# Optimization experiments

Measured on AMD Instinct MI355X. Metric: run time of the kernel, lower is better.

Reference implementation:

```python
import jax, jax.numpy as jnp
import numpy as np

TEMP = 0.1      # temperature
REG = 0.1       # ot_reg
MAX_ITER = 100  # Sinkhorn-style scaling iterations (original early-stops on tol; fixed-point is identical post-convergence)

B, D, N_PER = 64, 128, 512  # examples, embed dim, nodes/tokens per example


def _normalize(x):
    # torch F.normalize(dim=1): x / max(||x||, eps)
    n = jnp.linalg.norm(x, axis=1, keepdims=True)
    return x / jnp.maximum(n, 1e-12)


def setup_inputs() -> dict:
    key = jax.random.key(0)
    k0, k1, k2, k3 = jax.random.split(key, 4)
    N = B * N_PER
    return {
        "struct_global": jax.random.normal(k0, (B, D), jnp.float32),
        "seq_global": jax.random.normal(k1, (B, D), jnp.float32),
        "struct_nodes": jax.random.normal(k2, (N, D), jnp.float32),
        "seq_tokens": jax.random.normal(k3, (N, D), jnp.float32),
        # sorted, equal-size segments: example i owns rows [i*N_PER, (i+1)*N_PER)
        "batch_idx": jnp.repeat(jnp.arange(B), N_PER),
    }


def _global_nt_xent(struct_emb, seq_emb):
    s = _normalize(struct_emb)
    q = _normalize(seq_emb)
    sim = (s @ q.T) / TEMP                      # [B, B]
    loss_i = -jnp.mean(jnp.diagonal(jax.nn.log_softmax(sim, axis=1)))
    loss_j = -jnp.mean(jnp.diagonal(jax.nn.log_softmax(sim.T, axis=1)))
    return (loss_i + loss_j) / 2.0


def _local_ot_loss(struct_nodes, seq_tokens):
    # batch_idx is sorted equal-size segments -> dense batched reshape
    sn = _normalize(struct_nodes).reshape(B, N_PER, D)
    st = _normalize(seq_tokens).reshape(B, N_PER, D)
    C = -jnp.einsum('bnd,bmd->bnm', sn, st)     # [B, n, m] cost
    n = m = N_PER
    # Original detaches cost to numpy before OT -> transport plan P is a constant w.r.t. grads
    C_sg = jax.lax.stop_gradient(C)
    P0 = jnp.exp(-C_sg / REG)
    a = jnp.full((B, n), 1.0 / n, C.dtype)
    b = jnp.full((B, m), 1.0 / m, C.dtype)

    def body(_, uv):
        u, v = uv
        # Jacobi-style update: both use the previous (u, v), matching the source
        u_new = a / jnp.einsum('bnm,bm->bn', P0, v)
        v_new = b / jnp.einsum('bnm,bn->bm', P0, u)
        u_new = jnp.nan_to_num(u_new, nan=1.0 / n, posinf=1.0 / n, neginf=1.0 / n)
        v_new = jnp.nan_to_num(v_new, nan=1.0 / m, posinf=1.0 / m, neginf=1.0 / m)
        return (u_new, v_new)

    u, v = jax.lax.fori_loop(0, MAX_ITER, body, (a, b))  # init u=1/n, v=1/m as in source
    P = u[:, :, None] * P0 * v[:, None, :]      # diag(u) @ P0 @ diag(v)
    total = jnp.sum(P * C)                      # grads flow through C only
    return total / B


def reference(struct_global, seq_global, struct_nodes, seq_tokens, batch_idx):
    global_loss = _global_nt_xent(struct_global, seq_global)
    local_loss = _local_ot_loss(struct_nodes, seq_tokens)
    total_loss = global_loss + local_loss
    return (global_loss, local_loss, total_loss)
```

## Files before the change

kernel.cpp:

```cpp
#include <hip/hip_runtime.h>
#include <cstdint>
#include <cmath>

#define NB_EX 64
#define DIMD 128
#define NP 512
constexpr float MARG = 1.0f / 512.0f;

__device__ __forceinline__ float bf2f_lo(unsigned w) { return __uint_as_float(w << 16); }
__device__ __forceinline__ float bf2f_hi(unsigned w) { return __uint_as_float(w & 0xFFFF0000u); }
__device__ __forceinline__ unsigned short f2bf(float f) {
    unsigned u = __float_as_uint(f);
    u += 0x7FFFu + ((u >> 16) & 1u);
    return (unsigned short)(u >> 16);
}
__device__ __forceinline__ float wred64(float v) {
#pragma unroll
    for (int m = 1; m < 64; m <<= 1) v += __shfl_xor(v, m, 64);
    return v;
}

__device__ __forceinline__ unsigned l2_sc0_load(const unsigned* p) {
    unsigned v;
    asm volatile("global_load_dword %0, %1, off sc0\n\ts_waitcnt vmcnt(0)"
                 : "=v"(v) : "v"(p) : "memory");
    return v;
}

__device__ __forceinline__ int self_detect(const unsigned* probe, int t) {
    __shared__ int sd_cnt[4];
    unsigned w = probe[t];
    unsigned e = (w >> 7) & 0xFFu;
    unsigned long long m = __ballot(e >= 110u && e <= 130u);
    if ((t & 63) == 0) sd_cnt[t >> 6] = __popcll(m);
    __syncthreads();
    int c = sd_cnt[0] + sd_cnt[1] + sd_cnt[2] + sd_cnt[3];
    __syncthreads();
    return c >= 128;
}

#define O_SIMG   0
#define O_RNAN   16384
#define O_RNBN   147456
#define O_COLP   278528
#define O_COLPIF 2375680
#define O_P0     4472832

__global__ void k_rnormAB(const void* anr, const void* bnr, float* rnan, float* rnbn) {
    int t = threadIdx.x;
    int flag = self_detect((const unsigned*)anr, t);
    int gr  = blockIdx.x * 4 + (t >> 6);
    int lane = t & 63;
    const void* in = (gr < 32768) ? anr : bnr;
    float* rn      = (gr < 32768) ? rnan : rnbn;
    int row = gr & 32767;
    float f0, f1;
    if (flag) {
        unsigned w = ((const unsigned*)in)[row * 64 + lane];
        f0 = bf2f_lo(w); f1 = bf2f_hi(w);
    } else {
        float2 v = ((const float2*)in)[row * 64 + lane];
        f0 = v.x; f1 = v.y;
    }
    float ss = wred64(f0 * f0 + f1 * f1);
    if (lane == 0) rn[row] = 1.0f / fmaxf(sqrtf(ss), 1e-12f);
}

__global__ void k_simg(const void* sgr, const void* qgr, float* simg) {
    __shared__ float rls[128];
    int t = threadIdx.x;
    int flag = self_detect((const unsigned*)sgr, t);
    int w = t >> 6, lane = t & 63;
    for (int rr = 0; rr < 32; rr++) {
        int ri = w * 32 + rr;
        const void* base = (ri < 64) ? sgr : qgr;
        int row = ri & 63;
        float f0, f1;
        if (flag) {
            unsigned wd = ((const unsigned*)base)[row * 64 + lane];
            f0 = bf2f_lo(wd); f1 = bf2f_hi(wd);
        } else {
            float2 v = ((const float2*)base)[row * 64 + lane];
            f0 = v.x; f1 = v.y;
        }
        float ss = wred64(f0 * f0 + f1 * f1);
        if (lane == 0) rls[ri] = 1.0f / fmaxf(sqrtf(ss), 1e-12f);
    }
    __syncthreads();
    int g = blockIdx.x * 256 + t;
    int i = g >> 6, j = g & 63;
    float dot = 0.f;
    if (flag) {
        const unsigned* a = (const unsigned*)sgr + i * 64;
        const unsigned* b = (const unsigned*)qgr + j * 64;
        for (int k = 0; k < 64; k++) {
            unsigned wa = a[k], wb = b[k];
            dot += bf2f_lo(wa) * bf2f_lo(wb);
            dot += bf2f_hi(wa) * bf2f_hi(wb);
        }
    } else {
        const float4* a = (const float4*)sgr + i * 32;
        const float4* b = (const float4*)qgr + j * 32;
        for (int k = 0; k < 32; k++) {
            float4 x = a[k], y = b[k];
            dot += x.x * y.x + x.y * y.y + x.z * y.z + x.w * y.w;
        }
    }
    simg[g] = dot * rls[i] * rls[64 + j] * 10.0f;
}

__global__ void k_gloss(const float* __restrict__ simg, float* outf) {
    __shared__ float red[64];
    int i = threadIdx.x;
    if (i < 64) {
        float m = -1e30f;
        for (int j = 0; j < 64; j++) m = fmaxf(m, simg[i * 64 + j]);
        float se = 0.f;
        for (int j = 0; j < 64; j++) se += expf(simg[i * 64 + j] - m);
        float rl = simg[i * 64 + i] - (m + logf(se));
        float m2 = -1e30f;
        for (int j = 0; j < 64; j++) m2 = fmaxf(m2, simg[j * 64 + i]);
        float se2 = 0.f;
        for (int j = 0; j < 64; j++) se2 += expf(simg[j * 64 + i] - m2);
        float cl = simg[i * 64 + i] - (m2 + logf(se2));
        red[i] = rl + cl;
    }
    __syncthreads();
    if (i == 0) {
        float s = 0.f;
        for (int k = 0; k < 64; k++) s += red[k];
        float g = -s / 128.0f;
        outf[0] = g;
        outf[1] = 0.0f;
        outf[2] = g;
    }
}

__global__ void k_build(const void* anr, const void* bnr, const float* rnan, const float* rnbn,
                        unsigned short* p0) {
    int t  = threadIdx.x;
    int flag = self_detect((const unsigned*)anr, t);
    int b   = blockIdx.y;
    int r0t = (blockIdx.x >> 2) * 128;
    int c0t = (blockIdx.x & 3) * 128;
    __shared__ float As[128][33];
    __shared__ float Bs[128][33];
    int tr = t >> 4, tc = t & 15;
    float acc[8][8];
#pragma unroll
    for (int i = 0; i < 8; i++)
#pragma unroll
        for (int j = 0; j < 8; j++) acc[i][j] = 0.f;

    for (int kc = 0; kc < 4; kc++) {
        for (int ii = 0; ii < 4; ii++) {
            int idx = t + 256 * ii;
            int r = idx >> 3, c4 = idx & 7;
            {
                int grow = b * NP + r0t + r;
                float sc = rnan[grow];
                float f0, f1, f2, f3;
                if (flag) {
                    const unsigned* src = (const unsigned*)anr + ((grow * DIMD + kc * 32 + c4 * 4) >> 1);
                    unsigned w0 = src[0], w1 = src[1];
                    f0 = bf2f_lo(w0); f1 = bf2f_hi(w0); f2 = bf2f_lo(w1); f3 = bf2f_hi(w1);
                } else {
                    float4 v = *((const float4*)((const float*)anr + grow * DIMD + kc * 32 + c4 * 4));
                    f0 = v.x; f1 = v.y; f2 = v.z; f3 = v.w;
                }
                As[r][c4 * 4 + 0] = f0 * sc; As[r][c4 * 4 + 1] = f1 * sc;
                As[r][c4 * 4 + 2] = f2 * sc; As[r][c4 * 4 + 3] = f3 * sc;
            }
            {
                int grow = b * NP + c0t + r;
                float sc = rnbn[grow];
                float f0, f1, f2, f3;
                if (flag) {
                    const unsigned* src = (const unsigned*)bnr + ((grow * DIMD + kc * 32 + c4 * 4) >> 1);
                    unsigned w0 = src[0], w1 = src[1];
                    f0 = bf2f_lo(w0); f1 = bf2f_hi(w0); f2 = bf2f_lo(w1); f3 = bf2f_hi(w1);
                } else {
                    float4 v = *((const float4*)((const float*)bnr + grow * DIMD + kc * 32 + c4 * 4));
                    f0 = v.x; f1 = v.y; f2 = v.z; f3 = v.w;
                }
                Bs[r][c4 * 4 + 0] = f0 * sc; Bs[r][c4 * 4 + 1] = f1 * sc;
                Bs[r][c4 * 4 + 2] = f2 * sc; Bs[r][c4 * 4 + 3] = f3 * sc;
            }
        }
        __syncthreads();
        for (int kk = 0; kk < 32; kk++) {
            float av[8], bv[8];
#pragma unroll
            for (int i = 0; i < 8; i++) av[i] = As[tr * 8 + i][kk];
#pragma unroll
            for (int j = 0; j < 8; j++) bv[j] = Bs[tc * 8 + j][kk];
#pragma unroll
            for (int i = 0; i < 8; i++)
#pragma unroll
                for (int j = 0; j < 8; j++) acc[i][j] += av[i] * bv[j];
        }
        __syncthreads();
    }
#pragma unroll
    for (int i = 0; i < 8; i++) {
        int grow = b * NP + r0t + tr * 8 + i;
        unsigned short h[8];
#pragma unroll
        for (int j = 0; j < 8; j++) h[j] = f2bf(expf(acc[i][j] * 10.0f));
        uint4 pk;
        pk.x = (unsigned)h[0] | ((unsigned)h[1] << 16);
        pk.y = (unsigned)h[2] | ((unsigned)h[3] << 16);
        pk.z = (unsigned)h[4] | ((unsigned)h[5] << 16);
        pk.w = (unsigned)h[6] | ((unsigned)h[7] << 16);
        *((uint4*)(p0 + ((size_t)grow * NP + c0t + tc * 8))) = pk;
    }
}

__device__ __forceinline__ void store_dual(unsigned* l2p, unsigned* ifp, unsigned v) {
    *l2p = v;
    __hip_atomic_store(ifp, v, __ATOMIC_RELAXED, __HIP_MEMORY_SCOPE_AGENT);
}
__device__ __forceinline__ void poll_sums(const unsigned* crdL2, const unsigned* crdIF,
                                          unsigned tag, int col0, int col1,
                                          float& r0, float& r1) {
    unsigned got[8];
    unsigned need = 0xFFu;
    int round = 0;
    while (need) {
#pragma unroll
        for (int p = 0; p < 4; ++p) {
            unsigned m0 = 1u << p, m1 = 1u << (p + 4);
            if (need & m0) {
                unsigned g = (round < 4)
                    ? l2_sc0_load(crdL2 + (p << 9) + col0)
                    : __hip_atomic_load(crdIF + (p << 9) + col0, __ATOMIC_RELAXED,
                                        __HIP_MEMORY_SCOPE_AGENT);
                if ((g & 0xFFFFu) == tag) { got[p] = g; need &= ~m0; }
            }
            if (need & m1) {
                unsigned g = (round < 4)
                    ? l2_sc0_load(crdL2 + (p << 9) + col1)
                    : __hip_atomic_load(crdIF + (p << 9) + col1, __ATOMIC_RELAXED,
                                        __HIP_MEMORY_SCOPE_AGENT);
                if ((g & 0xFFFFu) == tag) { got[p + 4] = g; need &= ~m1; }
            }
        }
        if (need) __builtin_amdgcn_s_sleep(1);
        ++round;
    }
    r0 = 0.f; r1 = 0.f;
#pragma unroll
    for (int p = 0; p < 4; ++p) {
        r0 += __uint_as_float(got[p] & 0xFFFF0000u);
        r1 += __uint_as_float(got[p + 4] & 0xFFFF0000u);
    }
}

__global__ __launch_bounds__(256, 1) void k_persist(const unsigned short* __restrict__ p0,
                                                    unsigned* __restrict__ colpL2,
                                                    unsigned* __restrict__ colpIF,
                                                    float* __restrict__ outf) {
    int blk = blockIdx.x;
    int rb  = blk >> 6;
    int b   = blk & 63;
    int rowbase = rb * 128;
    int t = threadIdx.x, w = t >> 6, lane = t & 63;

    __shared__ float credU[4][512];
    __shared__ float credV[4][512];
    __shared__ float v_sU[512];
    __shared__ float v_sV[512];
    __shared__ float u_sU[128];
    __shared__ float u_sV[128];
    __shared__ float bs[4];

    uint4 pw[32];
#pragma unroll
    for (int r = 0; r < 32; r++) {
        int row = rowbase + w * 32 + r;
        pw[r] = ((const uint4*)(p0 + (((size_t)(b << 9) + row) << 9)))[lane];
    }
    int col0 = t, col1 = t + 256;
    if (t < 128) u_sU[t] = MARG;
    v_sV[col0] = MARG; v_sV[col1] = MARG;
    __syncthreads();

#pragma unroll 1
    for (int s = 0; s < 50; ++s) {
        unsigned tag = (unsigned)(s + 1);
        int bank = s & 1;
        {
            float ca[8];
#pragma unroll
            for (int k = 0; k < 8; ++k) ca[k] = 0.f;
#pragma unroll
            for (int r = 0; r < 32; ++r) {
                float u_r = u_sU[w * 32 + r];
                uint4 pv = pw[r];
                ca[0] += bf2f_lo(pv.x) * u_r; ca[1] += bf2f_hi(pv.x) * u_r;
                ca[2] += bf2f_lo(pv.y) * u_r; ca[3] += bf2f_hi(pv.y) * u_r;
                ca[4] += bf2f_lo(pv.z) * u_r; ca[5] += bf2f_hi(pv.z) * u_r;
                ca[6] += bf2f_lo(pv.w) * u_r; ca[7] += bf2f_hi(pv.w) * u_r;
            }
#pragma unroll
            for (int k = 0; k < 8; ++k) credU[w][lane * 8 + k] = ca[k];
        }
        __syncthreads();
        {
            int slot = ((bank * 64 + b) * 4 + rb) << 9;
            float s0 = credU[0][col0] + credU[1][col0] + credU[2][col0] + credU[3][col0];
            float s1 = credU[0][col1] + credU[1][col1] + credU[2][col1] + credU[3][col1];
            store_dual(colpL2 + slot + col0, colpIF + slot + col0,
                       ((unsigned)f2bf(s0) << 16) | tag);
            store_dual(colpL2 + slot + col1, colpIF + slot + col1,
                       ((unsigned)f2bf(s1) << 16) | tag);
        }
        {
            float vr[8];
#pragma unroll
            for (int k = 0; k < 8; ++k) vr[k] = v_sV[lane * 8 + k];
#pragma unroll
            for (int g = 0; g < 4; ++g) {
                float rp[8];
#pragma unroll
                for (int j = 0; j < 8; ++j) {
                    uint4 pv = pw[g * 8 + j];
                    rp[j] = bf2f_lo(pv.x) * vr[0] + bf2f_hi(pv.x) * vr[1]
                          + bf2f_lo(pv.y) * vr[2] + bf2f_hi(pv.y) * vr[3]
                          + bf2f_lo(pv.z) * vr[4] + bf2f_hi(pv.z) * vr[5]
                          + bf2f_lo(pv.w) * vr[6] + bf2f_hi(pv.w) * vr[7];
                }
#pragma unroll
                for (int m = 1; m < 64; m <<= 1)
#pragma unroll
                    for (int j = 0; j < 8; ++j) rp[j] += __shfl_xor(rp[j], m, 64);
                float sel = rp[0];
#pragma unroll
                for (int j = 1; j < 8; ++j) if (lane == j) sel = rp[j];
                if (lane < 8) {
                    float q = MARG / sel;
                    if (!isfinite(q)) q = MARG;
                    u_sV[w * 32 + g * 8 + lane] = q;
                }
            }
        }
        {
            float ca[8];
#pragma unroll
            for (int k = 0; k < 8; ++k) ca[k] = 0.f;
#pragma unroll
            for (int r = 0; r < 32; ++r) {
                float u_r = u_sV[w * 32 + r];
                uint4 pv = pw[r];
                ca[0] += bf2f_lo(pv.x) * u_r; ca[1] += bf2f_hi(pv.x) * u_r;
                ca[2] += bf2f_lo(pv.y) * u_r; ca[3] += bf2f_hi(pv.y) * u_r;
                ca[4] += bf2f_lo(pv.z) * u_r; ca[5] += bf2f_hi(pv.z) * u_r;
                ca[6] += bf2f_lo(pv.w) * u_r; ca[7] += bf2f_hi(pv.w) * u_r;
            }
#pragma unroll
            for (int k = 0; k < 8; ++k) credV[w][lane * 8 + k] = ca[k];
        }
        __syncthreads();
        {
            int base = ((bank * 64 + b) * 4) << 9;
            float r0, r1;
            poll_sums(colpL2 + base, colpIF + base, tag, col0, col1, r0, r1);
            float q0 = MARG / r0; if (!isfinite(q0)) q0 = MARG;
            float q1 = MARG / r1; if (!isfinite(q1)) q1 = MARG;
            v_sU[col0] = q0;
            v_sU[col1] = q1;
        }
        __syncthreads();
        {
            int slot = (((2 + bank) * 64 + b) * 4 + rb) << 9;
            float s0 = credV[0][col0] + credV[1][col0] + credV[2][col0] + credV[3][col0];
            float s1 = credV[0][col1] + credV[1][col1] + credV[2][col1] + credV[3][col1];
            store_dual(colpL2 + slot + col0, colpIF + slot + col0,
                       ((unsigned)f2bf(s0) << 16) | tag);
            store_dual(colpL2 + slot + col1, colpIF + slot + col1,
                       ((unsigned)f2bf(s1) << 16) | tag);
        }
        {
            float vr[8];
#pragma unroll
            for (int k = 0; k < 8; ++k) vr[k] = v_sU[lane * 8 + k];
#pragma unroll
            for (int g = 0; g < 4; ++g) {
                float rp[8];
#pragma unroll
                for (int j = 0; j < 8; ++j) {
                    uint4 pv = pw[g * 8 + j];
                    rp[j] = bf2f_lo(pv.x) * vr[0] + bf2f_hi(pv.x) * vr[1]
                          + bf2f_lo(pv.y) * vr[2] + bf2f_hi(pv.y) * vr[3]
                          + bf2f_lo(pv.z) * vr[4] + bf2f_hi(pv.z) * vr[5]
                          + bf2f_lo(pv.w) * vr[6] + bf2f_hi(pv.w) * vr[7];
                }
#pragma unroll
                for (int m = 1; m < 64; m <<= 1)
#pragma unroll
                    for (int j = 0; j < 8; ++j) rp[j] += __shfl_xor(rp[j], m, 64);
                float sel = rp[0];
#pragma unroll
                for (int j = 1; j < 8; ++j) if (lane == j) sel = rp[j];
                if (lane < 8) {
                    float q = MARG / sel;
                    if (!isfinite(q)) q = MARG;
                    u_sU[w * 32 + g * 8 + lane] = q;
                }
            }
        }
        {
            int base = (((2 + bank) * 64 + b) * 4) << 9;
            float r0, r1;
            poll_sums(colpL2 + base, colpIF + base, tag, col0, col1, r0, r1);
            float q0 = MARG / r0; if (!isfinite(q0)) q0 = MARG;
            float q1 = MARG / r1; if (!isfinite(q1)) q1 = MARG;
            v_sV[col0] = q0;
            v_sV[col1] = q1;
        }
        __syncthreads();
    }

    float vr[8];
#pragma unroll
    for (int k = 0; k < 8; ++k) vr[k] = v_sV[lane * 8 + k];
    float acc = 0.f;
#pragma unroll
    for (int r = 0; r < 32; ++r) {
        float u_r = u_sU[w * 32 + r];
        uint4 pv = pw[r];
        float f[8];
        f[0] = bf2f_lo(pv.x); f[1] = bf2f_hi(pv.x);
        f[2] = bf2f_lo(pv.y); f[3] = bf2f_hi(pv.y);
        f[4] = bf2f_lo(pv.z); f[5] = bf2f_hi(pv.z);
        f[6] = bf2f_lo(pv.w); f[7] = bf2f_hi(pv.w);
#pragma unroll
        for (int k = 0; k < 8; ++k) {
            float p = f[k];
            acc += u_r * p * vr[k] * (-0.1f) * logf(p);
        }
    }
    acc = wred64(acc);
    if (lane == 0) bs[w] = acc;
    __syncthreads();
    if (t == 0) {
        float c = (bs[0] + bs[1] + bs[2] + bs[3]) * (1.0f / 64.0f);
        atomicAdd(&outf[1], c);
        atomicAdd(&outf[2], c);
    }
}

extern "C" void kernel_launch(void* const* d_in, const int* in_sizes, int n_in,
                              void* d_out, int out_size, void* d_ws, size_t ws_size,
                              hipStream_t stream) {
    const void* sg = d_in[0];
    const void* qg = d_in[1];
    const void* an = d_in[2];
    const void* bn = d_in[3];
    char* ws = (char*)d_ws;
    float* outf = (float*)d_out;

    float* simg      = (float*)(ws + O_SIMG);
    float* rnan      = (float*)(ws + O_RNAN);
    float* rnbn      = (float*)(ws + O_RNBN);
    unsigned* colpL2 = (unsigned*)(ws + O_COLP);
    unsigned* colpIF = (unsigned*)(ws + O_COLPIF);
    unsigned short* p0 = (unsigned short*)(ws + O_P0);

    k_rnormAB<<<16384, 256, 0, stream>>>(an, bn, rnan, rnbn);
    k_simg<<<16, 256, 0, stream>>>(sg, qg, simg);
    k_gloss<<<1, 256, 0, stream>>>(simg, outf);
    k_build<<<dim3(16, 64), 256, 0, stream>>>(an, bn, rnan, rnbn, p0);
    k_persist<<<256, 256, 0, stream>>>(p0, colpL2, colpIF, outf);
}
```

Measured before the change: 754.5 us.

## Split each example across two 512-thread blocks to halve cross-block polling

The persistent Sinkhorn kernel now uses 128 blocks of 512 threads, each owning 256 rows of one example, instead of 256 blocks of 256 threads owning 128 rows. Each block computes its own column partial locally and polls only its single partner block rather than four peers. The polling routine is simplified to a per-thread single-slot wait. This cuts inter-block synchronization traffic and latency per half-iteration, at the cost of fewer active CUs and more work per block.

```diff
diff --git a/kernel.cpp b/kernel.cpp
--- a/kernel.cpp
+++ b/kernel.cpp
@@ -17,13 +17,6 @@
 __device__ __forceinline__ float wred64(float v) {
 #pragma unroll
     for (int m = 1; m < 64; m <<= 1) v += __shfl_xor(v, m, 64);
-    return v;
-}
-
-__device__ __forceinline__ unsigned l2_sc0_load(const unsigned* p) {
-    unsigned v;
-    asm volatile("global_load_dword %0, %1, off sc0\n\ts_waitcnt vmcnt(0)"
-                 : "=v"(v) : "v"(p) : "memory");
     return v;
 }
 
@@ -220,59 +213,40 @@
     *l2p = v;
     __hip_atomic_store(ifp, v, __ATOMIC_RELAXED, __HIP_MEMORY_SCOPE_AGENT);
 }
-__device__ __forceinline__ void poll_sums(const unsigned* crdL2, const unsigned* crdIF,
-                                          unsigned tag, int col0, int col1,
-                                          float& r0, float& r1) {
-    unsigned got[8];
-    unsigned need = 0xFFu;
-    int round = 0;
-    while (need) {
-#pragma unroll
-        for (int p = 0; p < 4; ++p) {
-            unsigned m0 = 1u << p, m1 = 1u << (p + 4);
-            if (need & m0) {
-                unsigned g = (round < 4)
-                    ? l2_sc0_load(crdL2 + (p << 9) + col0)
-                    : __hip_atomic_load(crdIF + (p << 9) + col0, __ATOMIC_RELAXED,
-                                        __HIP_MEMORY_SCOPE_AGENT);
-                if ((g & 0xFFFFu) == tag) { got[p] = g; need &= ~m0; }
-            }
-            if (need & m1) {
-                unsigned g = (round < 4)
-                    ? l2_sc0_load(crdL2 + (p << 9) + col1)
-                    : __hip_atomic_load(crdIF + (p << 9) + col1, __ATOMIC_RELAXED,
-                                        __HIP_MEMORY_SCOPE_AGENT);
-                if ((g & 0xFFFFu) == tag) { got[p + 4] = g; need &= ~m1; }
-            }
-        }
-        if (need) __builtin_amdgcn_s_sleep(1);
-        ++round;
-    }
-    r0 = 0.f; r1 = 0.f;
-#pragma unroll
-    for (int p = 0; p < 4; ++p) {
-        r0 += __uint_as_float(got[p] & 0xFFFF0000u);
-        r1 += __uint_as_float(got[p + 4] & 0xFFFF0000u);
-    }
-}
-
-__global__ __launch_bounds__(256, 1) void k_persist(const unsigned short* __restrict__ p0,
+
+__device__ __forceinline__ float poll_one(const unsigned* pL2, const unsigned* pIF, unsigned tag) {
+    unsigned q;
+#pragma unroll 1
+    for (int round = 0;; ++round) {
+        asm volatile("global_load_dword %0, %1, off sc0\n\ts_waitcnt vmcnt(0)"
+                     : "=v"(q) : "v"(pL2) : "memory");
+        if ((q & 0xFFFFu) == tag) break;
+        if (round >= 1) {
+            q = __hip_atomic_load(pIF, __ATOMIC_RELAXED, __HIP_MEMORY_SCOPE_AGENT);
+            if ((q & 0xFFFFu) == tag) break;
+            __builtin_amdgcn_s_sleep(1);
+        }
+    }
+    return __uint_as_float(q & 0xFFFF0000u);
+}
+
+__global__ __launch_bounds__(512, 2) void k_persist(const unsigned short* __restrict__ p0,
                                                     unsigned* __restrict__ colpL2,
                                                     unsigned* __restrict__ colpIF,
                                                     float* __restrict__ outf) {
     int blk = blockIdx.x;
     int rb  = blk >> 6;
     int b   = blk & 63;
-    int rowbase = rb * 128;
+    int rowbase = rb * 256;
     int t = threadIdx.x, w = t >> 6, lane = t & 63;
 
-    __shared__ float credU[4][512];
-    __shared__ float credV[4][512];
+    __shared__ float credU[8][512];
+    __shared__ float credV[8][512];
     __shared__ float v_sU[512];
     __shared__ float v_sV[512];
-    __shared__ float u_sU[128];
-    __shared__ float u_sV[128];
-    __shared__ float bs[4];
+    __shared__ float u_sU[256];
+    __shared__ float u_sV[256];
+    __shared__ float bs[8];
 
     uint4 pw[32];
 #pragma unroll
@@ -280,10 +254,11 @@
         int row = rowbase + w * 32 + r;
         pw[r] = ((const uint4*)(p0 + (((size_t)(b << 9) + row) << 9)))[lane];
     }
-    int col0 = t, col1 = t + 256;
-    if (t < 128) u_sU[t] = MARG;
-    v_sV[col0] = MARG; v_sV[col1] = MARG;
-    __syncthreads();
+    if (t < 256) u_sU[t] = MARG;
+    v_sV[t] = MARG;
+    __syncthreads();
+
+    float myU = 0.f, myV = 0.f;
 
 #pragma unroll 1
     for (int s = 0; s < 50; ++s) {
@@ -307,13 +282,12 @@
         }
         __syncthreads();
         {
-            int slot = ((bank * 64 + b) * 4 + rb) << 9;
-            float s0 = credU[0][col0] + credU[1][col0] + credU[2][col0] + credU[3][col0];
-            float s1 = credU[0][col1] + credU[1][col1] + credU[2][col1] + credU[3][col1];
-            store_dual(colpL2 + slot + col0, colpIF + slot + col0,
-                       ((unsigned)f2bf(s0) << 16) | tag);
-            store_dual(colpL2 + slot + col1, colpIF + slot + col1,
-                       ((unsigned)f2bf(s1) << 16) | tag);
+            int slot = (((0 * 2 + bank) * 64 + b) * 2 + rb) << 9;
+            float s0 = credU[0][t] + credU[1][t] + credU[2][t] + credU[3][t]
+                     + credU[4][t] + credU[5][t] + credU[6][t] + credU[7][t];
+            unsigned pk = ((unsigned)f2bf(s0) << 16) | tag;
+            store_dual(colpL2 + slot + t, colpIF + slot + t, pk);
+            myU = __uint_as_float(pk & 0xFFFF0000u);
         }
         {
             float vr[8];
@@ -362,23 +336,20 @@
         }
         __syncthreads();
         {
-            int base = ((bank * 64 + b) * 4) << 9;
-            float r0, r1;
-            poll_sums(colpL2 + base, colpIF + base, tag, col0, col1, r0, r1);
-            float q0 = MARG / r0; if (!isfinite(q0)) q0 = MARG;
-            float q1 = MARG / r1; if (!isfinite(q1)) q1 = MARG;
-            v_sU[col0] = q0;
-            v_sU[col1] = q1;
-        }
-        __syncthreads();
-        {
-            int slot = (((2 + bank) * 64 + b) * 4 + rb) << 9;
-            float s0 = credV[0][col0] + credV[1][col0] + credV[2][col0] + credV[3][col0];
-            float s1 = credV[0][col1] + credV[1][col1] + credV[2][col1] + credV[3][col1];
-            store_dual(colpL2 + slot + col0, colpIF + slot + col0,
-                       ((unsigned)f2bf(s0) << 16) | tag);
-            store_dual(colpL2 + slot + col1, colpIF + slot + col1,
-                       ((unsigned)f2bf(s1) << 16) | tag);
+            int pslot = (((0 * 2 + bank) * 64 + b) * 2 + (rb ^ 1)) << 9;
+            float theirs = poll_one(colpL2 + pslot + t, colpIF + pslot + t, tag);
+            float q = MARG / (myU + theirs);
+            if (!isfinite(q)) q = MARG;
+            v_sU[t] = q;
+        }
+        __syncthreads();
+        {
+            int slot = (((1 * 2 + bank) * 64 + b) * 2 + rb) << 9;
+            float s0 = credV[0][t] + credV[1][t] + credV[2][t] + credV[3][t]
+                     + credV[4][t] + credV[5][t] + credV[6][t] + credV[7][t];
+            unsigned pk = ((unsigned)f2bf(s0) << 16) | tag;
+            store_dual(colpL2 + slot + t, colpIF + slot + t, pk);
+            myV = __uint_as_float(pk & 0xFFFF0000u);
         }
         {
             float vr[8];
@@ -410,13 +381,11 @@
             }
         }
         {
-            int base = (((2 + bank) * 64 + b) * 4) << 9;
-            float r0, r1;
-            poll_sums(colpL2 + base, colpIF + base, tag, col0, col1, r0, r1);
-            float q0 = MARG / r0; if (!isfinite(q0)) q0 = MARG;
-            float q1 = MARG / r1; if (!isfinite(q1)) q1 = MARG;
-            v_sV[col0] = q0;
-            v_sV[col1] = q1;
+            int pslot = (((1 * 2 + bank) * 64 + b) * 2 + (rb ^ 1)) << 9;
+            float theirs = poll_one(colpL2 + pslot + t, colpIF + pslot + t, tag);
+            float q = MARG / (myV + theirs);
+            if (!isfinite(q)) q = MARG;
+            v_sV[t] = q;
         }
         __syncthreads();
     }
@@ -444,7 +413,7 @@
     if (lane == 0) bs[w] = acc;
     __syncthreads();
     if (t == 0) {
-        float c = (bs[0] + bs[1] + bs[2] + bs[3]) * (1.0f / 64.0f);
+        float c = (bs[0] + bs[1] + bs[2] + bs[3] + bs[4] + bs[5] + bs[6] + bs[7]) * (1.0f / 64.0f);
         atomicAdd(&outf[1], c);
         atomicAdd(&outf[2], c);
     }
@@ -471,5 +440,5 @@
     k_simg<<<16, 256, 0, stream>>>(sg, qg, simg);
     k_gloss<<<1, 256, 0, stream>>>(simg, outf);
     k_build<<<dim3(16, 64), 256, 0, stream>>>(an, bn, rnan, rnbn, p0);
-    k_persist<<<256, 256, 0, stream>>>(p0, colpL2, colpIF, outf);
-}
+    k_persist<<<128, 512, 0, stream>>>(p0, colpL2, colpIF, outf);
+}
```

New measurement: 1.313 ms. +74.0%, slower.
